# Optimization experiments

Hardware: AMD Instinct MI355X
Metric: run time of the kernel (lower is better)

## Reference

```python
import jax, jax.numpy as jnp
import numpy as np

T_SPCL = 0.05       # temperature_spcl
T_TMP = 0.1         # temperature_tmp
NUM_CLASSES = 8192  # fixed stand-in for labels.max()+1 (extra classes are empty -> masked out)
EPS = 1e-6

B, D, M = 128, 2048, 65536


def setup_inputs() -> dict:
    key = jax.random.key(0)
    k1, k2, k3, k4, k5, k6 = jax.random.split(key, 6)
    inputs = jax.random.normal(k1, (B, D), jnp.float32)
    feats_aug = jax.random.normal(k2, (B, 2, D), jnp.float32)
    feats_aug = feats_aug / jnp.linalg.norm(feats_aug, axis=-1, keepdims=True)
    idx = jax.random.randint(k3, (B,), 0, M)
    label = jax.random.randint(k4, (B,), 0, 32)
    features = jax.random.normal(k5, (M, D), jnp.float32)
    features = features / jnp.linalg.norm(features, axis=1, keepdims=True)  # bank stores normalized feats
    mem_labels = jax.random.randint(k6, (M,), 0, NUM_CLASSES)
    return dict(inputs=inputs, feats_aug=feats_aug, features=features,
                idx=idx, label=label, mem_labels=mem_labels)


def reference(inputs, feats_aug, features, idx, label, mem_labels):
    # ---- SPCL loss: memory-bank similarity + per-class segment mean + masked softmax ----
    x = inputs / jnp.linalg.norm(inputs, axis=1, keepdims=True)          # [B, D]
    sims = jnp.matmul(x, features.T) / T_SPCL                            # [B, M]
    # index_add over memory entries grouped by their pseudo-label
    sim = jax.ops.segment_sum(sims.T, mem_labels, num_segments=NUM_CLASSES)   # [C, B]
    nums = jax.ops.segment_sum(jnp.ones((M, 1), jnp.float32), mem_labels,
                               num_segments=NUM_CLASSES)                      # [C, 1]
    mask = (nums > 0).astype(jnp.float32)                                # [C, 1]
    sim = sim / (mask * nums + (1.0 - mask))                             # per-class mean sim
    exps = jnp.exp(sim.T) * mask.T                                       # [B, C] masked softmax (no max-shift, faithful)
    masked_sim = exps / (jnp.sum(exps, axis=1, keepdims=True) + EPS)
    targets = mem_labels[idx]                                            # [B]
    loss_spcl = -jnp.mean(jnp.log(masked_sim[jnp.arange(B), targets] + EPS))

    # ---- contrastive loss over two augmented views (world_size=1) ----
    f = jnp.concatenate([feats_aug[:, 0], feats_aug[:, 1]], axis=0)      # [2B, D]
    n2 = 2 * B
    logit_full = jnp.matmul(f, f.T)                                      # [2B, 2B]
    lab = label.reshape(-1, 1)
    lm = (lab == lab.T).astype(jnp.float32)                              # [B, B]
    lm = jnp.tile(lm, (2, 2))                                            # [2B, 2B]
    # drop the diagonal, keeping row order (masked_select equivalent)
    cols = jnp.arange(n2 - 1)[None, :]
    rows = jnp.arange(n2)[:, None]
    col_idx = cols + (cols >= rows).astype(cols.dtype)                   # [2B, 2B-1]
    L = jnp.take_along_axis(logit_full, col_idx, axis=1) / T_TMP         # [2B, 2B-1]
    pos_m = jnp.take_along_axis(lm, col_idx, axis=1)
    neg_m = 1.0 - pos_m
    # CE with label 0 over [pos, negs] = -pos + logsumexp([pos, negs]); stable shared max per row
    m = jnp.max(L, axis=1, keepdims=True)
    E = jnp.exp(L - m)
    neg_sum = jnp.sum(E * neg_m, axis=1, keepdims=True)                  # [2B, 1]
    per_pos = jnp.log(E + neg_sum) + m - L                               # loss for each candidate positive
    pos_cnt = jnp.sum(pos_m, axis=1)                                     # >= 1 (other view always positive)
    loss_contrastive = jnp.sum(jnp.sum(per_pos * pos_m, axis=1) / pos_cnt) / n2

    return loss_spcl + loss_contrastive
```

## Files before the change

### kernel.cpp

```cpp
#include <hip/hip_runtime.h>
#include <hip/hip_bf16.h>

#define Bdim 128
#define Ddim 2048
#define Mdim 65536
#define Cdim 8192
#define N2   256
#define T_SPCL_INV 20.0f
#define T_TMP_INV  10.0f

typedef __attribute__((ext_vector_type(8))) short  short8;
typedef __attribute__((ext_vector_type(4))) float  floatx4;

static __device__ __forceinline__ unsigned int pk2bf(float lo, float hi) {
  unsigned int a = __float_as_uint(lo);
  a += 0x7fffu + ((a >> 16) & 1u);
  unsigned int b = __float_as_uint(hi);
  b += 0x7fffu + ((b >> 16) & 1u);
  return (a >> 16) | (b & 0xffff0000u);
}

__global__ __launch_bounds__(256) void k_normalize(const float* __restrict__ in,
                                                   unsigned short* __restrict__ xbf) {
  __shared__ float red[4];
  int b = blockIdx.x, t = threadIdx.x;
  const float4* row = (const float4*)(in + (long)b * Ddim);
  float4 v0 = row[t * 2], v1 = row[t * 2 + 1];
  float ss = v0.x*v0.x + v0.y*v0.y + v0.z*v0.z + v0.w*v0.w
           + v1.x*v1.x + v1.y*v1.y + v1.z*v1.z + v1.w*v1.w;
  for (int off = 32; off; off >>= 1) ss += __shfl_down(ss, off);
  if ((t & 63) == 0) red[t >> 6] = ss;
  __syncthreads();
  float rn = rsqrtf(red[0] + red[1] + red[2] + red[3]);
  uint4 o;
  o.x = pk2bf(v0.x * rn, v0.y * rn);
  o.y = pk2bf(v0.z * rn, v0.w * rn);
  o.z = pk2bf(v1.x * rn, v1.y * rn);
  o.w = pk2bf(v1.z * rn, v1.w * rn);
  ((uint4*)(xbf + (long)b * Ddim))[t] = o;
}

__global__ __launch_bounds__(256) void k_castf(const float* __restrict__ fa,
                                               unsigned short* __restrict__ fbf) {
  int j = blockIdx.x, t = threadIdx.x;
  const float4* src = (const float4*)(fa + (long)((j & 127) * 2 + (j >> 7)) * Ddim);
  float4 v0 = src[t * 2], v1 = src[t * 2 + 1];
  uint4 o;
  o.x = pk2bf(v0.x, v0.y); o.y = pk2bf(v0.z, v0.w);
  o.z = pk2bf(v1.x, v1.y); o.w = pk2bf(v1.z, v1.w);
  ((uint4*)(fbf + (long)j * Ddim))[t] = o;
}

__global__ void k_count(const int* __restrict__ lab, int* __restrict__ counts) {
  int m = blockIdx.x * 256 + threadIdx.x;
  atomicAdd(&counts[lab[m]], 1);
}

__global__ __launch_bounds__(256) void k_prefix(const int* __restrict__ counts,
                                                int* __restrict__ offs,
                                                int* __restrict__ cursor) {
  __shared__ int lds[256];
  int t = threadIdx.x;
  int base = t * 32;
  int local[32];
  int s = 0;
#pragma unroll
  for (int i = 0; i < 32; ++i) { local[i] = counts[base + i]; s += local[i]; }
  lds[t] = s;
  __syncthreads();
  for (int off = 1; off < 256; off <<= 1) {
    int v = (t >= off) ? lds[t - off] : 0;
    __syncthreads();
    lds[t] += v;
    __syncthreads();
  }
  int run = lds[t] - s;
#pragma unroll
  for (int i = 0; i < 32; ++i) {
    offs[base + i] = run;
    cursor[base + i] = run;
    run += local[i];
  }
}

__global__ void k_scatter(const int* __restrict__ lab, int* __restrict__ cursor,
                          int* __restrict__ sorted) {
  int m = blockIdx.x * 256 + threadIdx.x;
  int p = atomicAdd(&cursor[lab[m]], 1);
  sorted[p] = m;
}

__global__ __launch_bounds__(256) void k_gemm(const float* __restrict__ feats,
                                              const unsigned short* __restrict__ xbf,
                                              float* __restrict__ sims) {
  __shared__ __align__(16) unsigned short aT[64 * 40];
  __shared__ __align__(16) unsigned short xT[128 * 40];
  int t = threadIdx.x;
  int lane = t & 63, wid = t >> 6;
  long m0 = (long)blockIdx.x * 64;

  int arow = t >> 2, aseg = t & 3;
  const float* gA = feats + (m0 + arow) * Ddim + aseg * 8;
  unsigned short* lA = &aT[arow * 40 + aseg * 8];

  int xrow = t >> 1, xhalf = t & 1;
  const unsigned short* gX = xbf + (long)xrow * Ddim + xhalf * 16;
  unsigned short* lX = &xT[xrow * 40 + xhalf * 16];

  const unsigned short* aF = &aT[(wid * 16 + (lane & 15)) * 40 + (lane >> 4) * 8];
  int bbase = (lane & 15) * 40 + (lane >> 4) * 8;

  floatx4 zero = {0.f, 0.f, 0.f, 0.f};
  floatx4 acc[8];
#pragma unroll
  for (int i = 0; i < 8; ++i) acc[i] = zero;

  for (int kt = 0; kt < Ddim / 32; ++kt) {
    int k0 = kt * 32;
    float4 f0 = *(const float4*)(gA + k0);
    float4 f1 = *(const float4*)(gA + k0 + 4);
    uint4 x0 = *(const uint4*)(gX + k0);
    uint4 x1 = *(const uint4*)(gX + k0 + 8);
    __syncthreads();
    uint4 pa;
    pa.x = pk2bf(f0.x, f0.y); pa.y = pk2bf(f0.z, f0.w);
    pa.z = pk2bf(f1.x, f1.y); pa.w = pk2bf(f1.z, f1.w);
    *(uint4*)lA = pa;
    *(uint4*)lX = x0;
    *(uint4*)(lX + 8) = x1;
    __syncthreads();
    short8 af = *(const short8*)aF;
#pragma unroll
    for (int nt = 0; nt < 8; ++nt) {
      short8 bf = *(const short8*)&xT[nt * 16 * 40 + bbase];
      acc[nt] = __builtin_amdgcn_mfma_f32_16x16x32_bf16(af, bf, acc[nt], 0, 0, 0);
    }
  }

  long orow = m0 + wid * 16 + (lane >> 4) * 4;
  int ocol = lane & 15;
#pragma unroll
  for (int nt = 0; nt < 8; ++nt) {
#pragma unroll
    for (int r = 0; r < 4; ++r) {
      sims[(orow + r) * Bdim + nt * 16 + ocol] = acc[nt][r] * T_SPCL_INV;
    }
  }
}

__global__ __launch_bounds__(256) void k_classmean(const float* __restrict__ sims,
                                                   const int* __restrict__ counts,
                                                   const int* __restrict__ offs,
                                                   const int* __restrict__ sorted,
                                                   float* __restrict__ exps) {
  int wid = threadIdx.x >> 6, lane = threadIdx.x & 63;
  int c = blockIdx.x * 4 + wid;
  int cnt = counts[c], off = offs[c];
  float sx = 0.f, sy = 0.f;
  for (int i = 0; i < cnt; ++i) {
    int m = sorted[off + i];
    float2 v = ((const float2*)(sims + (long)m * Bdim))[lane];
    sx += v.x; sy += v.y;
  }
  float2 e;
  if (cnt > 0) {
    float ic = (float)cnt;
    e.x = expf(sx / ic);
    e.y = expf(sy / ic);
  } else {
    e.x = 0.f; e.y = 0.f;
  }
  ((float2*)(exps + (long)c * Bdim))[lane] = e;
}

__global__ __launch_bounds__(128) void k_denom(const float* __restrict__ exps,
                                               float* __restrict__ denom) {
  int b = threadIdx.x;
  long c0 = (long)blockIdx.x * 128;
  float s = 0.f;
  for (int i = 0; i < 128; ++i) s += exps[(c0 + i) * Bdim + b];
  atomicAdd(&denom[b], s);
}

__global__ __launch_bounds__(128) void k_spcl(const float* __restrict__ exps,
                                              const float* __restrict__ denom,
                                              const int* __restrict__ idx,
                                              const int* __restrict__ mlab,
                                              float* __restrict__ out) {
  __shared__ float red[2];
  int b = threadIdx.x;
  int tc = mlab[idx[b]];
  float p = exps[(long)tc * Bdim + b] / (denom[b] + 1e-6f);
  float l = -logf(p + 1e-6f);
  for (int off = 32; off; off >>= 1) l += __shfl_down(l, off);
  if ((b & 63) == 0) red[b >> 6] = l;
  __syncthreads();
  if (b == 0) atomicAdd(out, (red[0] + red[1]) * (1.0f / Bdim));
}

__global__ __launch_bounds__(256) void k_logits(const unsigned short* __restrict__ fbf,
                                                float* __restrict__ logit) {
  int lane = threadIdx.x & 63, wid = threadIdx.x >> 6;
  int tm = blockIdx.x >> 2;
  int tn = (blockIdx.x & 3) * 4 + wid;
  const unsigned short* pA = fbf + (long)(tm * 16 + (lane & 15)) * Ddim + (lane >> 4) * 8;
  const unsigned short* pB = fbf + (long)(tn * 16 + (lane & 15)) * Ddim + (lane >> 4) * 8;
  floatx4 acc = {0.f, 0.f, 0.f, 0.f};
#pragma unroll 4
  for (int kt = 0; kt < 64; ++kt) {
    short8 a = *(const short8*)(pA + kt * 32);
    short8 b = *(const short8*)(pB + kt * 32);
    acc = __builtin_amdgcn_mfma_f32_16x16x32_bf16(a, b, acc, 0, 0, 0);
  }
  int r0 = tm * 16 + (lane >> 4) * 4;
  int c = tn * 16 + (lane & 15);
#pragma unroll
  for (int r = 0; r < 4; ++r) logit[(r0 + r) * N2 + c] = acc[r];
}

__global__ __launch_bounds__(256) void k_contrast(const float* __restrict__ logit,
                                                  const int* __restrict__ label,
                                                  float* __restrict__ out) {
  __shared__ float red[4];
  int i = blockIdx.x, j = threadIdx.x;
  int lane = j & 63, wid = j >> 6;
  float Lj = logit[i * N2 + j] * T_TMP_INV;
  bool self = (j == i);
  bool pos = (!self) && (label[i & 127] == label[j & 127]);

  float v = self ? -1e30f : Lj;
  for (int off = 32; off; off >>= 1) v = fmaxf(v, __shfl_down(v, off));
  if (lane == 0) red[wid] = v;
  __syncthreads();
  float m = fmaxf(fmaxf(red[0], red[1]), fmaxf(red[2], red[3]));
  __syncthreads();

  float E = self ? 0.f : expf(Lj - m);
  float neg = pos ? 0.f : E;
  for (int off = 32; off; off >>= 1) neg += __shfl_down(neg, off);
  if (lane == 0) red[wid] = neg;
  __syncthreads();
  float neg_sum = red[0] + red[1] + red[2] + red[3];
  __syncthreads();

  float pp = pos ? (logf(E + neg_sum) + m - Lj) : 0.f;
  for (int off = 32; off; off >>= 1) pp += __shfl_down(pp, off);
  if (lane == 0) red[wid] = pp;
  __syncthreads();
  float s_pp = red[0] + red[1] + red[2] + red[3];
  __syncthreads();

  float cw = pos ? 1.f : 0.f;
  for (int off = 32; off; off >>= 1) cw += __shfl_down(cw, off);
  if (lane == 0) red[wid] = cw;
  __syncthreads();
  float s_cnt = red[0] + red[1] + red[2] + red[3];

  if (j == 0) atomicAdd(out, (s_pp / s_cnt) * (1.0f / N2));
}

extern "C" void kernel_launch(void* const* d_in, const int* in_sizes, int n_in,
                              void* d_out, int out_size, void* d_ws, size_t ws_size,
                              hipStream_t stream) {
  const float* inputs     = (const float*)d_in[0];
  const float* feats_aug  = (const float*)d_in[1];
  const float* features   = (const float*)d_in[2];
  const int*   idx        = (const int*)d_in[3];
  const int*   label      = (const int*)d_in[4];
  const int*   mem_labels = (const int*)d_in[5];
  float* out = (float*)d_out;

  char* w = (char*)d_ws;
  auto alloc = [&](size_t bytes) {
    char* p = w;
    w += (bytes + 511) & ~((size_t)511);
    return p;
  };
  unsigned short* xbf    = (unsigned short*)alloc((size_t)Bdim * Ddim * 2);
  unsigned short* fbf    = (unsigned short*)alloc((size_t)N2 * Ddim * 2);
  int*   counts = (int*)alloc(Cdim * 4);
  int*   offs   = (int*)alloc(Cdim * 4);
  int*   cursor = (int*)alloc(Cdim * 4);
  int*   sorted = (int*)alloc(Mdim * 4);
  float* denom  = (float*)alloc(Bdim * 4);
  float* logit  = (float*)alloc(N2 * N2 * 4);
  float* exps   = (float*)alloc((size_t)Cdim * Bdim * 4);
  float* sims   = (float*)alloc((size_t)Mdim * Bdim * 4);

  hipMemsetAsync(counts, 0, Cdim * 4, stream);
  hipMemsetAsync(denom, 0, Bdim * 4, stream);
  hipMemsetAsync(out, 0, (size_t)out_size * sizeof(float), stream);

  k_normalize<<<Bdim, 256, 0, stream>>>(inputs, xbf);
  k_castf<<<N2, 256, 0, stream>>>(feats_aug, fbf);
  k_count<<<Mdim / 256, 256, 0, stream>>>(mem_labels, counts);
  k_prefix<<<1, 256, 0, stream>>>(counts, offs, cursor);
  k_scatter<<<Mdim / 256, 256, 0, stream>>>(mem_labels, cursor, sorted);
  k_gemm<<<Mdim / 64, 256, 0, stream>>>(features, xbf, sims);
  k_classmean<<<Cdim / 4, 256, 0, stream>>>(sims, counts, offs, sorted, exps);
  k_denom<<<Cdim / 128, 128, 0, stream>>>(exps, denom);
  k_spcl<<<1, Bdim, 0, stream>>>(exps, denom, idx, mem_labels, out);
  k_logits<<<64, 256, 0, stream>>>(fbf, logit);
  k_contrast<<<N2, 256, 0, stream>>>(logit, label, out);
}
```

Baseline: 805.2 us.

## Enlarge GEMM tile to 128 rows with register prefetch of next K slice

```diff
diff --git a/kernel.cpp b/kernel.cpp
--- a/kernel.cpp
+++ b/kernel.cpp
@@ -59,13 +59,17 @@
 __global__ __launch_bounds__(256) void k_prefix(const int* __restrict__ counts,
                                                 int* __restrict__ offs,
                                                 int* __restrict__ cursor) {
+  __shared__ int sc[Cdim];
   __shared__ int lds[256];
   int t = threadIdx.x;
+#pragma unroll
+  for (int i = 0; i < 32; ++i) sc[i * 256 + t] = counts[i * 256 + t];
+  __syncthreads();
   int base = t * 32;
   int local[32];
   int s = 0;
 #pragma unroll
-  for (int i = 0; i < 32; ++i) { local[i] = counts[base + i]; s += local[i]; }
+  for (int i = 0; i < 32; ++i) { local[i] = sc[base + i]; s += local[i]; }
   lds[t] = s;
   __syncthreads();
   for (int off = 1; off < 256; off <<= 1) {
@@ -90,60 +94,84 @@
   sorted[p] = m;
 }
 
+#define LDSW 72
 __global__ __launch_bounds__(256) void k_gemm(const float* __restrict__ feats,
                                               const unsigned short* __restrict__ xbf,
                                               float* __restrict__ sims) {
-  __shared__ __align__(16) unsigned short aT[64 * 40];
-  __shared__ __align__(16) unsigned short xT[128 * 40];
+  __shared__ __align__(16) unsigned short aT[128 * LDSW];
+  __shared__ __align__(16) unsigned short xT[128 * LDSW];
   int t = threadIdx.x;
   int lane = t & 63, wid = t >> 6;
-  long m0 = (long)blockIdx.x * 64;
-
-  int arow = t >> 2, aseg = t & 3;
-  const float* gA = feats + (m0 + arow) * Ddim + aseg * 8;
-  unsigned short* lA = &aT[arow * 40 + aseg * 8];
-
-  int xrow = t >> 1, xhalf = t & 1;
-  const unsigned short* gX = xbf + (long)xrow * Ddim + xhalf * 16;
-  unsigned short* lX = &xT[xrow * 40 + xhalf * 16];
-
-  const unsigned short* aF = &aT[(wid * 16 + (lane & 15)) * 40 + (lane >> 4) * 8];
-  int bbase = (lane & 15) * 40 + (lane >> 4) * 8;
+  long m0 = (long)blockIdx.x * 128;
+
+  int srow = t >> 1, shalf = t & 1;
+  const float*          gA = feats + (m0 + srow) * Ddim + shalf * 32;
+  const unsigned short* gX = xbf + (long)srow * Ddim + shalf * 32;
+  unsigned short* lA = &aT[srow * LDSW + shalf * 32];
+  unsigned short* lX = &xT[srow * LDSW + shalf * 32];
+
+  int abase0 = (wid * 32 + (lane & 15)) * LDSW + (lane >> 4) * 8;
+  int abase1 = abase0 + 16 * LDSW;
+  int bbase  = (lane & 15) * LDSW + (lane >> 4) * 8;
 
   floatx4 zero = {0.f, 0.f, 0.f, 0.f};
-  floatx4 acc[8];
-#pragma unroll
-  for (int i = 0; i < 8; ++i) acc[i] = zero;
-
-  for (int kt = 0; kt < Ddim / 32; ++kt) {
-    int k0 = kt * 32;
-    float4 f0 = *(const float4*)(gA + k0);
-    float4 f1 = *(const float4*)(gA + k0 + 4);
-    uint4 x0 = *(const uint4*)(gX + k0);
-    uint4 x1 = *(const uint4*)(gX + k0 + 8);
+  floatx4 acc[2][8];
+#pragma unroll
+  for (int mr = 0; mr < 2; ++mr)
+#pragma unroll
+    for (int nt = 0; nt < 8; ++nt) acc[mr][nt] = zero;
+
+  float4 ra[8];
+  uint4  rx[4];
+#pragma unroll
+  for (int i = 0; i < 8; ++i) ra[i] = ((const float4*)gA)[i];
+#pragma unroll
+  for (int i = 0; i < 4; ++i) rx[i] = ((const uint4*)gX)[i];
+
+  for (int kt = 0; kt < Ddim / 64; ++kt) {
     __syncthreads();
-    uint4 pa;
-    pa.x = pk2bf(f0.x, f0.y); pa.y = pk2bf(f0.z, f0.w);
-    pa.z = pk2bf(f1.x, f1.y); pa.w = pk2bf(f1.z, f1.w);
-    *(uint4*)lA = pa;
-    *(uint4*)lX = x0;
-    *(uint4*)(lX + 8) = x1;
+#pragma unroll
+    for (int i = 0; i < 4; ++i) {
+      uint4 w;
+      w.x = pk2bf(ra[2*i].x, ra[2*i].y);
+      w.y = pk2bf(ra[2*i].z, ra[2*i].w);
+      w.z = pk2bf(ra[2*i+1].x, ra[2*i+1].y);
+      w.w = pk2bf(ra[2*i+1].z, ra[2*i+1].w);
+      ((uint4*)lA)[i] = w;
+      ((uint4*)lX)[i] = rx[i];
+    }
+    if (kt + 1 < Ddim / 64) {
+      const float*          nA = gA + (kt + 1) * 64;
+      const unsigned short* nX = gX + (kt + 1) * 64;
+#pragma unroll
+      for (int i = 0; i < 8; ++i) ra[i] = ((const float4*)nA)[i];
+#pragma unroll
+      for (int i = 0; i < 4; ++i) rx[i] = ((const uint4*)nX)[i];
+    }
     __syncthreads();
-    short8 af = *(const short8*)aF;
+#pragma unroll
+    for (int kk = 0; kk < 2; ++kk) {
+      short8 a0 = *(const short8*)&aT[abase0 + kk * 32];
+      short8 a1 = *(const short8*)&aT[abase1 + kk * 32];
+#pragma unroll
+      for (int nt = 0; nt < 8; ++nt) {
+        short8 b = *(const short8*)&xT[bbase + nt * 16 * LDSW + kk * 32];
+        acc[0][nt] = __builtin_amdgcn_mfma_f32_16x16x32_bf16(a0, b, acc[0][nt], 0, 0, 0);
+        acc[1][nt] = __builtin_amdgcn_mfma_f32_16x16x32_bf16(a1, b, acc[1][nt], 0, 0, 0);
+      }
+    }
+  }
+
+  int ocol = lane & 15;
+#pragma unroll
+  for (int mr = 0; mr < 2; ++mr) {
+    long orow = m0 + wid * 32 + mr * 16 + (lane >> 4) * 4;
 #pragma unroll
     for (int nt = 0; nt < 8; ++nt) {
-      short8 bf = *(const short8*)&xT[nt * 16 * 40 + bbase];
-      acc[nt] = __builtin_amdgcn_mfma_f32_16x16x32_bf16(af, bf, acc[nt], 0, 0, 0);
-    }
-  }
-
-  long orow = m0 + wid * 16 + (lane >> 4) * 4;
-  int ocol = lane & 15;
-#pragma unroll
-  for (int nt = 0; nt < 8; ++nt) {
-#pragma unroll
-    for (int r = 0; r < 4; ++r) {
-      sims[(orow + r) * Bdim + nt * 16 + ocol] = acc[nt][r] * T_SPCL_INV;
+#pragma unroll
+      for (int r = 0; r < 4; ++r) {
+        sims[(orow + r) * Bdim + nt * 16 + ocol] = acc[mr][nt][r] * T_SPCL_INV;
+      }
     }
   }
 }
@@ -164,9 +192,9 @@
   }
   float2 e;
   if (cnt > 0) {
-    float ic = (float)cnt;
-    e.x = expf(sx / ic);
-    e.y = expf(sy / ic);
+    float ic = 1.0f / (float)cnt;
+    e.x = expf(sx * ic);
+    e.y = expf(sy * ic);
   } else {
     e.x = 0.f; e.y = 0.f;
   }
@@ -178,6 +206,7 @@
   int b = threadIdx.x;
   long c0 = (long)blockIdx.x * 128;
   float s = 0.f;
+#pragma unroll 8
   for (int i = 0; i < 128; ++i) s += exps[(c0 + i) * Bdim + b];
   atomicAdd(&denom[b], s);
 }
@@ -206,7 +235,7 @@
   const unsigned short* pA = fbf + (long)(tm * 16 + (lane & 15)) * Ddim + (lane >> 4) * 8;
   const unsigned short* pB = fbf + (long)(tn * 16 + (lane & 15)) * Ddim + (lane >> 4) * 8;
   floatx4 acc = {0.f, 0.f, 0.f, 0.f};
-#pragma unroll 4
+#pragma unroll 8
   for (int kt = 0; kt < 64; ++kt) {
     short8 a = *(const short8*)(pA + kt * 32);
     short8 b = *(const short8*)(pB + kt * 32);
@@ -296,7 +325,7 @@
   k_count<<<Mdim / 256, 256, 0, stream>>>(mem_labels, counts);
   k_prefix<<<1, 256, 0, stream>>>(counts, offs, cursor);
   k_scatter<<<Mdim / 256, 256, 0, stream>>>(mem_labels, cursor, sorted);
-  k_gemm<<<Mdim / 64, 256, 0, stream>>>(features, xbf, sims);
+  k_gemm<<<Mdim / 128, 256, 0, stream>>>(features, xbf, sims);
   k_classmean<<<Cdim / 4, 256, 0, stream>>>(sims, counts, offs, sorted, exps);
   k_denom<<<Cdim / 128, 128, 0, stream>>>(exps, denom);
   k_spcl<<<1, Bdim, 0, stream>>>(exps, denom, idx, mem_labels, out);
```

Result: no change. 815.1 us (+1.2%).
